# Optimization experiments

Hardware: AMD Instinct MI355X
Metric: run time of the kernel (lower is better)

Reference implementation:

```python
import jax, jax.numpy as jnp
import numpy as np

B = 256
H = W = 14
HW = H * W
TS = 0.03  # sigmoid temperature
TC = 0.07  # contrastive temperature
TP_K = int(HW * 0.1)   # 19
TN_K = int(HW * 0.5)   # 98
EPS_NORM = 1e-12
EPS_PD = 1e-6  # torch F.pairwise_distance eps


def _l2norm(x, axis):
    n = jnp.sqrt(jnp.sum(x * x, axis=axis, keepdims=True))
    return x / jnp.maximum(n, EPS_NORM)


def _conv(x, w):
    return jax.lax.conv_general_dilated(
        x, w, window_strides=(1, 1), padding='SAME',
        dimension_numbers=('NCHW', 'OIHW', 'NCHW'))


def setup_inputs() -> dict:
    key = jax.random.key(0)
    ks = jax.random.split(key, 7)
    ev = jax.random.normal(ks[0], (B, 384, H, W), dtype=jnp.float32)
    ea = jax.random.normal(ks[1], (B, 2048), dtype=jnp.float32)
    masks = jax.random.randint(ks[2], (B, H, W), 0, 2).astype(jnp.int32)
    masks = masks.at[:, 0, 0].set(1)  # guarantee nonzero mask area
    W_fc1 = jax.random.normal(ks[3], (512, 2048), dtype=jnp.float32) * 0.02
    W_fc2 = jax.random.normal(ks[4], (512, 512), dtype=jnp.float32) * 0.02
    W_conv1 = jax.random.normal(ks[5], (512, 384, 3, 3), dtype=jnp.float32) * 0.02
    W_conv2 = jax.random.normal(ks[6], (512, 512, 3, 3), dtype=jnp.float32) * 0.02
    return {'ev': ev, 'ea': ea, 'masks': masks, 'W_fc1': W_fc1,
            'W_fc2': W_fc2, 'W_conv1': W_conv1, 'W_conv2': W_conv2}


def reference(ev, ea, masks, W_fc1, W_fc2, W_conv1, W_conv2):
    # Audio_Proj: fc2(relu(fc1(ea)))  -> (B, 512)
    fa = jnp.maximum(ea @ W_fc1.T, 0.0) @ W_fc2.T

    # Visual_Proj: conv2(relu(conv1(ev))) -> (B, 512, 14, 14)
    fv_map = _conv(jnp.maximum(_conv(ev, W_conv1), 0.0), W_conv2)
    fv_map_norm = _l2norm(fv_map, axis=1)

    # masked mean pooling over the Ncut mask -> indicator vector (B, 512)
    m = masks.astype(jnp.float32)
    ind_vec = jnp.sum(fv_map * m[:, None], axis=(2, 3)) / jnp.sum(m, axis=(1, 2))[:, None]
    ind_vec_norm = _l2norm(ind_vec, axis=1)

    # Sij[i, j, p] = <fv_map_norm[i, :, p], ind_vec_norm[j]>  -> (B, B, HW)
    Sij = jnp.einsum('ichw,jc->ijhw', fv_map_norm, ind_vec_norm).reshape(B, B, HW)

    # per-row topk thresholds (kth largest / kth smallest)
    pos_thr = jax.lax.top_k(Sij, TP_K)[0][..., -1:]           # (B, B, 1)
    neg_thr = -jax.lax.top_k(-Sij, TN_K)[0][..., -1:]         # (B, B, 1)

    m_p = jax.nn.sigmoid((Sij - pos_thr) / TS)
    m_n = 1.0 - jax.nn.sigmoid((Sij - neg_thr) / TS)

    SP = jnp.sum(Sij * m_p, axis=-1) / jnp.sum(m_p, axis=-1)  # (B, B)
    SN = jnp.sum(Sij * m_n, axis=-1) / jnp.sum(m_n, axis=-1)  # (B, B)

    logits1 = jnp.concatenate([SP, SN], axis=1) / TC          # (B, 2B)
    logits2 = jnp.concatenate([SP.T, SN.T], axis=1) / TC
    labels = jnp.arange(B)
    loss1 = -jnp.mean(jax.nn.log_softmax(logits1, axis=-1)[labels, labels])
    loss2 = -jnp.mean(jax.nn.log_softmax(logits2, axis=-1)[labels, labels])

    # squared pairwise distance between detached ind_vec and fa (torch eps in diff)
    diff = jax.lax.stop_gradient(ind_vec)[:, None, :] - fa[None, :, :] + EPS_PD
    dist_mat = jnp.sum(diff * diff, axis=-1)                  # (B, B)

    ivn_d = jax.lax.stop_gradient(ind_vec_norm)
    vv_logits = ivn_d @ ivn_d.T
    eye = jnp.eye(B, dtype=jnp.float32)
    w = -vv_logits * (1.0 - eye) + eye
    dist_mat = dist_mat * w

    mask_mat = eye - (1.0 - eye) / (B - 1)
    loss3 = jnp.mean(jnp.maximum(jnp.sum(dist_mat * mask_mat, axis=1) + 0.6, 0.0))
    loss4 = jnp.mean(jnp.maximum(jnp.sum(dist_mat * mask_mat, axis=0) + 0.6, 0.0))

    return ((loss1 + loss2) / 2.0, (loss3 + loss4) / 2.0)
```

## Files before the change

### kernel.cpp

```cpp
#include <hip/hip_runtime.h>
#include <stdint.h>


typedef __attribute__((ext_vector_type(8))) short bf16x8;
typedef __attribute__((ext_vector_type(4))) float f32x4;

__device__ __forceinline__ unsigned short f2bf(float x) {
  unsigned u = __float_as_uint(x);
  unsigned r = u + 0x7FFFu + ((u >> 16) & 1u);
  return (unsigned short)(r >> 16);
}
__device__ __forceinline__ float bf2f(unsigned short h) {
  return __uint_as_float(((unsigned)h) << 16);
}

typedef const __attribute__((address_space(1))) void* gptr1_t;
typedef __attribute__((address_space(3))) void* lptr3_t;
__device__ __forceinline__ void gload_lds16(const void* g, void* l) {
  __builtin_amdgcn_global_load_lds((gptr1_t)g, (lptr3_t)l, 16, 0, 0);
}

__device__ __forceinline__ float waveSum(float v) {
#pragma unroll
  for (int m = 1; m < 64; m <<= 1) v += __shfl_xor(v, m, 64);
  return v;
}
__device__ __forceinline__ float waveMax(float v) {
#pragma unroll
  for (int m = 1; m < 64; m <<= 1) v = fmaxf(v, __shfl_xor(v, m, 64));
  return v;
}
template <int NW>
__device__ __forceinline__ float blockSum(float v) {
  __shared__ float sh[NW];
  v = waveSum(v);
  int wv = threadIdx.x >> 6, ln = threadIdx.x & 63;
  if (ln == 0) sh[wv] = v;
  __syncthreads();
  float r = 0.f;
#pragma unroll
  for (int w = 0; w < NW; ++w) r += sh[w];
  __syncthreads();
  return r;
}
template <int NW>
__device__ __forceinline__ float blockMax(float v) {
  __shared__ float sh[NW];
  v = waveMax(v);
  int wv = threadIdx.x >> 6, ln = threadIdx.x & 63;
  if (ln == 0) sh[wv] = v;
  __syncthreads();
  float r = -3.4e38f;
#pragma unroll
  for (int w = 0; w < NW; ++w) r = fmaxf(r, sh[w]);
  __syncthreads();
  return r;
}

#define RA 65536

template <int KC, int EPI>
__global__ __launch_bounds__(256, 2) void convtap6_k(
    const unsigned short* __restrict__ A, const unsigned short* __restrict__ Bw,
    unsigned short* __restrict__ C) {
  __shared__ __align__(16) short Ah[256 * 72];
  __shared__ __align__(16) short Bb[2][128 * 72];
  const int tid = threadIdx.x;
  const int wave = tid >> 6, lane = tid & 63;
  const int wm = wave >> 1, wn = wave & 1;
  const int quad = lane >> 4, tq = lane & 15;
  const int img = blockIdx.x, n0 = blockIdx.y * 128;

  int pab[7];
#pragma unroll
  for (int mi = 0; mi < 7; ++mi) {
    int p = wm * 112 + mi * 16 + tq;
    int h = p / 14, w = p - h * 14;
    int pr = (p < 196) ? ((h + 1) * 16 + w + 1) : 17;
    pab[mi] = pr * 72 + quad * 8;
  }
  int nb[4];
#pragma unroll
  for (int ni = 0; ni < 4; ++ni)
    nb[ni] = (wn * 64 + ni * 16 + tq) * 72 + quad * 8;

  const char* Ab = (const char*)A;
  const char* Bg = (const char*)Bw;
  const int l16 = lane * 16;

  f32x4 acc[7][4];
#pragma unroll
  for (int mi = 0; mi < 7; ++mi)
#pragma unroll
    for (int ni = 0; ni < 4; ++ni) {
      f32x4 z = {0.f, 0.f, 0.f, 0.f};
      acc[mi][ni] = z;
    }

  auto stageA = [&](int kc) {
    size_t s0 = ((size_t)kc * RA + img * 256) * 144;
#pragma unroll
    for (int i = 0; i < 9; ++i) {
      int c = wave + i * 4;
      gload_lds16(Ab + s0 + (size_t)c * 1024 + l16, (char*)Ah + c * 1024);
    }
  };
  auto stageB = [&](int t, int kc, int buf) {
    size_t s0 = ((size_t)(t * KC + kc) * 512 + n0) * 144;
#pragma unroll
    for (int i = 0; i < 5; ++i) {
      int c = wave + i * 4;
      if (c < 18)
        gload_lds16(Bg + s0 + (size_t)c * 1024 + l16, (char*)Bb[buf] + c * 1024);
    }
  };

  stageA(0);
  stageB(0, 0, 0);
  __syncthreads();

  const int NS = KC * 9;
#pragma unroll 1
  for (int s = 0; s < NS; ++s) {
    int kc = s / 9, t = s - kc * 9;
    if (s + 1 < NS) {
      int kc1 = (s + 1) / 9, t1 = (s + 1) - kc1 * 9;
      stageB(t1, kc1, (s + 1) & 1);
    }
    const int aoff = (((t / 3) - 1) * 16 + (t % 3) - 1) * 72;
    const short* Bc = Bb[s & 1];
#pragma unroll
    for (int h = 0; h < 2; ++h) {
      bf16x8 af[7], bf[4];
#pragma unroll
      for (int mi = 0; mi < 7; ++mi)
        af[mi] = *(const bf16x8*)&Ah[pab[mi] + aoff + h * 32];
#pragma unroll
      for (int ni = 0; ni < 4; ++ni)
        bf[ni] = *(const bf16x8*)&Bc[nb[ni] + h * 32];
#pragma unroll
      for (int mi = 0; mi < 7; ++mi)
#pragma unroll
        for (int ni = 0; ni < 4; ++ni)
          acc[mi][ni] = __builtin_amdgcn_mfma_f32_16x16x32_bf16(
              af[mi], bf[ni], acc[mi][ni], 0, 0, 0);
    }
    __syncthreads();
    if (t == 8 && kc + 1 < KC) {
      stageA(kc + 1);
      __syncthreads();
    }
  }

#pragma unroll
  for (int mi = 0; mi < 7; ++mi) {
#pragma unroll
    for (int r = 0; r < 4; ++r) {
      int p = wm * 112 + mi * 16 + quad * 4 + r;
      if (p >= 196) continue;
      int h = p / 14, w = p - h * 14;
      if (EPI == 0) {
        int cell = img * 256 + (h + 1) * 16 + w + 1;
        int slice = (n0 >> 6) + wn;
        size_t ob = ((size_t)slice * RA + cell) * 72 + tq;
#pragma unroll
        for (int ni = 0; ni < 4; ++ni)
          C[ob + ni * 16] = f2bf(fmaxf(acc[mi][ni][r], 0.f));
      } else {
        size_t ob = (size_t)(img * 196 + p) * 512 + n0 + wn * 64 + tq;
#pragma unroll
        for (int ni = 0; ni < 4; ++ni)
          C[ob + ni * 16] = f2bf(acc[mi][ni][r]);
      }
    }
  }
}

template <int K, int NLD, int EPI>
__global__ __launch_bounds__(256, 2) void gemm1_k(
    const unsigned short* __restrict__ A, const unsigned short* __restrict__ Bw,
    void* __restrict__ C, const float* __restrict__ rs) {
  __shared__ short As[128 * 64];
  __shared__ short Bs[128 * 64];
  const int tid = threadIdx.x;
  const int wave = tid >> 6, lane = tid & 63;
  const int m0 = blockIdx.x * 128, n0 = blockIdx.y * 128;
  const int rr8 = lane >> 3, seg = lane & 7, gseg = seg ^ rr8;
  const int wm = wave >> 1, wn = wave & 1;
  const int quad = lane >> 4, tq = lane & 15;

  size_t asrc[4], bsrc[4];
#pragma unroll
  for (int i8 = 0; i8 < 4; ++i8) {
    int rloc = wave * 32 + i8 * 8 + rr8;
    asrc[i8] = (size_t)(m0 + rloc) * K + gseg * 8;
    bsrc[i8] = (size_t)(n0 + rloc) * K + gseg * 8;
  }

  f32x4 acc[4][4];
#pragma unroll
  for (int mi = 0; mi < 4; ++mi)
#pragma unroll
    for (int ni = 0; ni < 4; ++ni) {
      f32x4 z = {0.f, 0.f, 0.f, 0.f};
      acc[mi][ni] = z;
    }

#pragma unroll 1
  for (int kc2 = 0; kc2 < K / 64; ++kc2) {
    int kb = kc2 * 64;
    __syncthreads();
#pragma unroll
    for (int i8 = 0; i8 < 4; ++i8) {
      gload_lds16(A + asrc[i8] + kb, &As[(wave * 32 + i8 * 8) * 64]);
      gload_lds16(Bw + bsrc[i8] + kb, &Bs[(wave * 32 + i8 * 8) * 64]);
    }
    __syncthreads();
#pragma unroll
    for (int h = 0; h < 2; ++h) {
      bf16x8 af[4], bfr[4];
#pragma unroll
      for (int mi = 0; mi < 4; ++mi) {
        int row = wm * 64 + mi * 16 + tq;
        af[mi] = *(const bf16x8*)&As[row * 64 +
                                     ((((h << 2) | quad) ^ (row & 7)) << 3)];
      }
#pragma unroll
      for (int ni = 0; ni < 4; ++ni) {
        int row = wn * 64 + ni * 16 + tq;
        bfr[ni] = *(const bf16x8*)&Bs[row * 64 +
                                      ((((h << 2) | quad) ^ (row & 7)) << 3)];
      }
#pragma unroll
      for (int mi = 0; mi < 4; ++mi)
#pragma unroll
        for (int ni = 0; ni < 4; ++ni)
          acc[mi][ni] = __builtin_amdgcn_mfma_f32_16x16x32_bf16(
              af[mi], bfr[ni], acc[mi][ni], 0, 0, 0);
    }
  }

#pragma unroll
  for (int mi = 0; mi < 4; ++mi) {
#pragma unroll
    for (int r = 0; r < 4; ++r) {
      int m = m0 + wm * 64 + mi * 16 + quad * 4 + r;
      float sc = (EPI == 3) ? rs[m] : 1.f;
      size_t obase = (size_t)m * NLD + n0 + wn * 64 + tq;
#pragma unroll
      for (int ni = 0; ni < 4; ++ni) {
        float v = acc[mi][ni][r];
        size_t idx = obase + ni * 16;
        if (EPI == 0)
          ((unsigned short*)C)[idx] = f2bf(fmaxf(v, 0.f));
        else if (EPI == 2)
          ((float*)C)[idx] = v;
        else
          ((float*)C)[idx] = v * sc;
      }
    }
  }
}

__global__ __launch_bounds__(256, 2) void gemm_xv_k(
    const unsigned short* __restrict__ ivpb, const unsigned short* __restrict__ fab,
    const unsigned short* __restrict__ indnb, float* __restrict__ Xm,
    float* __restrict__ Vm) {
  const unsigned short* A = blockIdx.z ? indnb : ivpb;
  const unsigned short* Bw = blockIdx.z ? indnb : fab;
  float* C = blockIdx.z ? Vm : Xm;
  __shared__ short As[128 * 64];
  __shared__ short Bs[128 * 64];
  const int tid = threadIdx.x;
  const int wave = tid >> 6, lane = tid & 63;
  const int m0 = blockIdx.x * 128, n0 = blockIdx.y * 128;
  const int rr8 = lane >> 3, seg = lane & 7, gseg = seg ^ rr8;
  const int wm = wave >> 1, wn = wave & 1;
  const int quad = lane >> 4, tq = lane & 15;
  size_t asrc[4], bsrc[4];
#pragma unroll
  for (int i8 = 0; i8 < 4; ++i8) {
    int rloc = wave * 32 + i8 * 8 + rr8;
    asrc[i8] = (size_t)(m0 + rloc) * 512 + gseg * 8;
    bsrc[i8] = (size_t)(n0 + rloc) * 512 + gseg * 8;
  }
  f32x4 acc[4][4];
#pragma unroll
  for (int mi = 0; mi < 4; ++mi)
#pragma unroll
    for (int ni = 0; ni < 4; ++ni) {
      f32x4 z = {0.f, 0.f, 0.f, 0.f};
      acc[mi][ni] = z;
    }
#pragma unroll 1
  for (int kc2 = 0; kc2 < 8; ++kc2) {
    int kb = kc2 * 64;
    __syncthreads();
#pragma unroll
    for (int i8 = 0; i8 < 4; ++i8) {
      gload_lds16(A + asrc[i8] + kb, &As[(wave * 32 + i8 * 8) * 64]);
      gload_lds16(Bw + bsrc[i8] + kb, &Bs[(wave * 32 + i8 * 8) * 64]);
    }
    __syncthreads();
#pragma unroll
    for (int h = 0; h < 2; ++h) {
      bf16x8 af[4], bfr[4];
#pragma unroll
      for (int mi = 0; mi < 4; ++mi) {
        int row = wm * 64 + mi * 16 + tq;
        af[mi] = *(const bf16x8*)&As[row * 64 +
                                     ((((h << 2) | quad) ^ (row & 7)) << 3)];
      }
#pragma unroll
      for (int ni = 0; ni < 4; ++ni) {
        int row = wn * 64 + ni * 16 + tq;
        bfr[ni] = *(const bf16x8*)&Bs[row * 64 +
                                      ((((h << 2) | quad) ^ (row & 7)) << 3)];
      }
#pragma unroll
      for (int mi = 0; mi < 4; ++mi)
#pragma unroll
        for (int ni = 0; ni < 4; ++ni)
          acc[mi][ni] = __builtin_amdgcn_mfma_f32_16x16x32_bf16(
              af[mi], bfr[ni], acc[mi][ni], 0, 0, 0);
    }
  }
#pragma unroll
  for (int mi = 0; mi < 4; ++mi)
#pragma unroll
    for (int r = 0; r < 4; ++r) {
      int m = m0 + wm * 64 + mi * 16 + quad * 4 + r;
      size_t obase = (size_t)m * 256 + n0 + wn * 64 + tq;
#pragma unroll
      for (int ni = 0; ni < 4; ++ni) C[obase + ni * 16] = acc[mi][ni][r];
    }
}

__global__ void prep_all_k(const float* __restrict__ ea,
                           const float* __restrict__ Wf1,
                           const float* __restrict__ Wf2,
                           const float* __restrict__ Wc1,
                           const float* __restrict__ Wc2,
                           unsigned short* __restrict__ eab,
                           unsigned short* __restrict__ wf1b,
                           unsigned short* __restrict__ wf2b,
                           unsigned short* __restrict__ wb1,
                           unsigned short* __restrict__ wb2,
                           unsigned int* __restrict__ x1u) {
  int i = blockIdx.x * 256 + threadIdx.x;
  if (i < 524288) {
    eab[i] = f2bf(ea[i]);
  } else if (i < 1572864) {
    int j = i - 524288;
    wf1b[j] = f2bf(Wf1[j]);
  } else if (i < 1835008) {
    int j = i - 1572864;
    wf2b[j] = f2bf(Wf2[j]);
  } else if (i < 3604480) {
    int j = i - 1835008;
    int t = j / (6 * 512 * 64), r = j - t * (6 * 512 * 64);
    int kc = r / (512 * 64), r2 = r - kc * (512 * 64);
    int n = r2 >> 6, c = r2 & 63;
    wb1[((size_t)(t * 6 + kc) * 512 + n) * 72 + c] =
        f2bf(Wc1[(n * 384 + kc * 64 + c) * 9 + t]);
  } else if (i < 5963776) {
    int j = i - 3604480;
    int t = j / (8 * 512 * 64), r = j - t * (8 * 512 * 64);
    int kc = r / (512 * 64), r2 = r - kc * (512 * 64);
    int n = r2 >> 6, c = r2 & 63;
    wb2[((size_t)(t * 8 + kc) * 512 + n) * 72 + c] =
        f2bf(Wc2[(n * 512 + kc * 64 + c) * 9 + t]);
  } else {
    int j = i - 5963776;
    int hr = j >> 8, u = j & 255;
    int slice = u >> 5, uu = u & 31;
    int b = hr / 60, c = hr - b * 60;
    int cell;
    if (c < 16) cell = c;
    else if (c < 32) cell = 240 + (c - 16);
    else if (c < 46) cell = (c - 31) * 16;
    else cell = (c - 45) * 16 + 15;
    x1u[((size_t)slice * RA + b * 256 + cell) * 36 + uu] = 0u;
  }
}

__global__ __launch_bounds__(256) void evpad_k(const float* __restrict__ ev,
                                               unsigned short* __restrict__ out) {
  int b = blockIdx.x, ct = blockIdx.y;
  __shared__ float tile[64][197];
  int tid = threadIdx.x;
  const float* src = ev + ((size_t)b * 384 + ct * 64) * 196;
#pragma unroll 1
  for (int it = 0; it < 49; ++it) {
    int idx = it * 256 + tid;
    int c = idx / 196, p = idx - c * 196;
    tile[c][p] = src[idx];
  }
  __syncthreads();
  unsigned short* dst = out + ((size_t)ct * RA + b * 256) * 72;
#pragma unroll 1
  for (int it = 0; it < 64; ++it) {
    int idx = it * 256 + tid;
    int cell = idx >> 6, c = idx & 63;
    int h = (cell >> 4) - 1, w = (cell & 15) - 1;
    float v = ((unsigned)h < 14u && (unsigned)w < 14u) ? tile[c][h * 14 + w]
                                                       : 0.f;
    dst[(size_t)cell * 72 + c] = f2bf(v);
  }
}


__global__ __launch_bounds__(512) void pool_k(
    const unsigned short* __restrict__ fv, const int* __restrict__ masks,
    unsigned short* __restrict__ indnb, unsigned short* __restrict__ ivpb,
    float* __restrict__ Pi, float* __restrict__ rn) {
  int b = blockIdx.x;
  int w = threadIdx.x >> 6, lane = threadIdx.x & 63;
  __shared__ float red[8][512];
  __shared__ float msh[8];
  float acc[8] = {0.f, 0.f, 0.f, 0.f, 0.f, 0.f, 0.f, 0.f};
  float msum = 0.f;
  for (int p = w; p < 196; p += 8) {
    float m = (float)masks[b * 196 + p];
    msum += m;
    uint4 d = *(const uint4*)(fv + (size_t)(b * 196 + p) * 512 + lane * 8);
    const unsigned short* hp = (const unsigned short*)&d;
    float ss = 0.f;
#pragma unroll
    for (int k = 0; k < 8; ++k) {
      float x = bf2f(hp[k]);
      ss += x * x;
      acc[k] += m * x;
    }
    ss = waveSum(ss);
    if (lane == 0) rn[b * 196 + p] = 1.f / fmaxf(sqrtf(ss), 1e-12f);
  }
#pragma unroll
  for (int k = 0; k < 8; ++k) red[w][lane * 8 + k] = acc[k];
  if (lane == 0) msh[w] = msum;
  __syncthreads();
  int tid = threadIdx.x;
  float s = 0.f, mtot = 0.f;
#pragma unroll
  for (int ww = 0; ww < 8; ++ww) {
    s += red[ww][tid];
    mtot += msh[ww];
  }
  float v = s / mtot;
  float ss2 = blockSum<8>(v * v);
  float sc = 1.f / fmaxf(sqrtf(ss2), 1e-12f);
  indnb[b * 512 + tid] = f2bf(v * sc);
  float ve = v + 1e-6f;
  ivpb[b * 512 + tid] = f2bf(ve);
  float p2 = blockSum<8>(ve * ve);
  if (tid == 0) Pi[b] = p2;
}

__global__ __launch_bounds__(512) void fanorm_k(const float* __restrict__ fa,
                                                unsigned short* __restrict__ fab,
                                                float* __restrict__ Qj) {
  int b = blockIdx.x, tid = threadIdx.x;
  float v = fa[b * 512 + tid];
  fab[b * 512 + tid] = f2bf(v);
  float q = blockSum<8>(v * v);
  if (tid == 0) Qj[b] = q;
}


__device__ __forceinline__ float radix_kth(unsigned k0, unsigned k1, unsigned k2,
                                           unsigned k3, int k) {
  unsigned prefix = 0;
  int kk = k;
#pragma unroll 1
  for (int bit = 31; bit >= 14; --bit) {
    unsigned thi = (prefix >> bit) | 1u;
    int c = __popcll(__ballot((k0 >> bit) == thi)) +
            __popcll(__ballot((k1 >> bit) == thi)) +
            __popcll(__ballot((k2 >> bit) == thi)) +
            __popcll(__ballot((k3 >> bit) == thi));
    if (kk <= c)
      prefix |= (1u << bit);
    else
      kk -= c;
  }
  unsigned u = (prefix & 0x80000000u) ? (prefix ^ 0x80000000u) : ~prefix;
  return __uint_as_float(u);
}
__device__ __forceinline__ unsigned sortkey(float x) {
  unsigned u = __float_as_uint(x);
  return u ^ (((int)u >> 31) | 0x80000000u);
}

__global__ __launch_bounds__(256) void spsn_k(const float* __restrict__ Sij,
                                              float* __restrict__ SP,
                                              float* __restrict__ SN) {
  int i = blockIdx.x, jg = blockIdx.y;
  int tid = threadIdx.x, wave = tid >> 6, lane = tid & 63;
  __shared__ float tile[196 * 65];
#pragma unroll 1
  for (int it = 0; it < 49; ++it) {
    int lin = it * 256 + tid;
    int p = lin >> 6, j = lin & 63;
    tile[p * 65 + j] = Sij[(size_t)(i * 196 + p) * 256 + jg * 64 + j];
  }
  __syncthreads();
#pragma unroll 1
  for (int jj = 0; jj < 16; ++jj) {
    int j = jj * 4 + wave;
    float v0 = tile[lane * 65 + j];
    float v1 = tile[(lane + 64) * 65 + j];
    float v2 = tile[(lane + 128) * 65 + j];
    bool val3 = lane < 4;
    float v3 = val3 ? tile[(lane + 192) * 65 + j] : 0.f;
    unsigned k0 = sortkey(v0), k1 = sortkey(v1), k2 = sortkey(v2);
    unsigned k3 = val3 ? sortkey(v3) : 0u;
    float thrP = radix_kth(k0, k1, k2, k3, 19);
    float thrN = radix_kth(k0, k1, k2, k3, 99);
    float spn = 0.f, spd = 0.f, snn = 0.f, snd = 0.f;
    const float invTS = 1.f / 0.03f;
#pragma unroll
    for (int q = 0; q < 4; ++q) {
      float v = (q == 0) ? v0 : (q == 1) ? v1 : (q == 2) ? v2 : v3;
      bool ok = (q < 3) || val3;
      if (ok) {
        float mp = 1.f / (1.f + __expf((thrP - v) * invTS));
        float mn = 1.f / (1.f + __expf((v - thrN) * invTS));
        spn += v * mp;
        spd += mp;
        snn += v * mn;
        snd += mn;
      }
    }
    spn = waveSum(spn); spd = waveSum(spd);
    snn = waveSum(snn); snd = waveSum(snd);
    if (lane == 0) {
      SP[i * 256 + jg * 64 + j] = spn / spd;
      SN[i * 256 + jg * 64 + j] = snn / snd;
    }
  }
}

__global__ __launch_bounds__(256) void loss12_k(const float* __restrict__ SP,
                                                const float* __restrict__ SN,
                                                float* __restrict__ out) {
  int r = blockIdx.x;
  int i = r & 255;
  bool col = r >= 256;
  int tid = threadIdx.x;
  const float invTC = 1.f / 0.07f;
  float a = (col ? SP[tid * 256 + i] : SP[i * 256 + tid]) * invTC;
  float b = (col ? SN[tid * 256 + i] : SN[i * 256 + tid]) * invTC;
  float mx = blockMax<4>(fmaxf(a, b));
  float se = blockSum<4>(__expf(a - mx) + __expf(b - mx));
  float lse = mx + __logf(se);
  if (tid == 0) {
    float diag = SP[i * 256 + i] * invTC;
    atomicAdd(out, -(diag - lse) * (1.f / 512.f));
  }
}

__global__ __launch_bounds__(256) void distcomb_k(
    const float* __restrict__ Pi, const float* __restrict__ Qj,
    const float* __restrict__ X, const float* __restrict__ V,
    float* __restrict__ val, float* __restrict__ out) {
  int i = blockIdx.x, j = threadIdx.x;
  float d = Pi[i] - 2.f * X[i * 256 + j] + Qj[j];
  float w = (i == j) ? 1.f : -V[i * 256 + j];
  float x = d * w;
  val[i * 256 + j] = x;
  __shared__ float diag_sh;
  if (j == i) diag_sh = x;
  float tot = blockSum<4>(x);
  if (j == 0) {
    float rs = diag_sh - (tot - diag_sh) * (1.f / 255.f);
    atomicAdd(out + 1, fmaxf(rs + 0.6f, 0.f) * (1.f / 512.f));
  }
}

__global__ __launch_bounds__(256) void loss4_k(const float* __restrict__ val,
                                               float* __restrict__ out) {
  int j = blockIdx.x, i = threadIdx.x;
  float x = val[i * 256 + j];
  __shared__ float diag_sh;
  if (i == j) diag_sh = x;
  float tot = blockSum<4>(x);
  if (i == 0) {
    float cs = diag_sh - (tot - diag_sh) * (1.f / 255.f);
    atomicAdd(out + 1, fmaxf(cs + 0.6f, 0.f) * (1.f / 512.f));
  }
}


extern "C" void kernel_launch(void* const* d_in, const int* in_sizes, int n_in,
                              void* d_out, int out_size, void* d_ws,
                              size_t ws_size, hipStream_t stream) {
  (void)in_sizes; (void)n_in; (void)out_size; (void)ws_size;
  const float* ev = (const float*)d_in[0];
  const float* ea = (const float*)d_in[1];
  const int* msk = (const int*)d_in[2];
  const float* Wf1 = (const float*)d_in[3];
  const float* Wf2 = (const float*)d_in[4];
  const float* Wc1 = (const float*)d_in[5];
  const float* Wc2 = (const float*)d_in[6];
  float* out = (float*)d_out;
  char* ws = (char*)d_ws;

  size_t off = 0;
  auto alloc = [&](size_t bytes) {
    void* p = ws + off;
    off = (off + bytes + 255) & ~(size_t)255;
    return p;
  };
  unsigned short* evb = (unsigned short*)alloc((size_t)6 * RA * 144);
  unsigned short* fv = evb;
  unsigned short* x1b = (unsigned short*)alloc((size_t)8 * RA * 144);
  float* Sij = (float*)x1b;
  unsigned short* wb1 = (unsigned short*)alloc((size_t)9 * 6 * 512 * 144);
  unsigned short* wb2 = (unsigned short*)alloc((size_t)9 * 8 * 512 * 144);
  unsigned short* eab = (unsigned short*)alloc((size_t)256 * 2048 * 2);
  unsigned short* wf1b = (unsigned short*)alloc((size_t)512 * 2048 * 2);
  unsigned short* wf2b = (unsigned short*)alloc((size_t)512 * 512 * 2);
  unsigned short* hb = (unsigned short*)alloc((size_t)256 * 512 * 2);
  float* fa = (float*)alloc((size_t)256 * 512 * 4);
  unsigned short* indnb = (unsigned short*)alloc((size_t)256 * 512 * 2);
  unsigned short* ivpb = (unsigned short*)alloc((size_t)256 * 512 * 2);
  unsigned short* fab = (unsigned short*)alloc((size_t)256 * 512 * 2);
  float* Pi = (float*)alloc(256 * 4);
  float* Qj = (float*)alloc(256 * 4);
  float* Xm = (float*)alloc((size_t)256 * 256 * 4);
  float* Vm = (float*)alloc((size_t)256 * 256 * 4);
  float* rn = (float*)alloc((size_t)50176 * 4);
  float* SP = (float*)alloc((size_t)256 * 256 * 4);
  float* SN = (float*)alloc((size_t)256 * 256 * 4);
  float* val = (float*)alloc((size_t)256 * 256 * 4);

  hipMemsetAsync(out, 0, 2 * sizeof(float), stream);

  prep_all_k<<<38656, 256, 0, stream>>>(ea, Wf1, Wf2, Wc1, Wc2, eab, wf1b,
                                        wf2b, wb1, wb2, (unsigned int*)x1b);
  evpad_k<<<dim3(256, 6), 256, 0, stream>>>(ev, evb);

  convtap6_k<6, 0><<<dim3(256, 4), 256, 0, stream>>>(evb, wb1, x1b);
  gemm1_k<2048, 512, 0><<<dim3(2, 4), 256, 0, stream>>>(eab, wf1b, hb, nullptr);
  gemm1_k<512, 512, 2><<<dim3(2, 4), 256, 0, stream>>>(hb, wf2b, fa, nullptr);
  convtap6_k<8, 1><<<dim3(256, 4), 256, 0, stream>>>(x1b, wb2, fv);

  pool_k<<<256, 512, 0, stream>>>(fv, msk, indnb, ivpb, Pi, rn);
  fanorm_k<<<256, 512, 0, stream>>>(fa, fab, Qj);

  gemm1_k<512, 256, 3><<<dim3(392, 2), 256, 0, stream>>>(fv, indnb, Sij, rn);
  gemm_xv_k<<<dim3(2, 2, 2), 256, 0, stream>>>(ivpb, fab, indnb, Xm, Vm);

  spsn_k<<<dim3(256, 4), 256, 0, stream>>>(Sij, SP, SN);
  loss12_k<<<512, 256, 0, stream>>>(SP, SN, out);
  distcomb_k<<<256, 256, 0, stream>>>(Pi, Qj, Xm, Vm, val, out);
  loss4_k<<<256, 256, 0, stream>>>(val, out);
}
```

Before: 852.0 us.

## Load conv weight fragments directly into registers and use padded-row M indexing

The conv kernels stop staging weight tiles through double-buffered LDS. Each wave now reads its B fragments straight from global memory into a two-slot register buffer, prefetching the next tap while the current one computes, and the weight layout is packed to 64 columns. The M dimension now indexes padded 16-wide rows directly, which removes the per-pixel div/mod and computes 224 rows instead of 196, with columns 14 and 15 skipped at output. This removes most per-tap barriers and frees LDS, at the cost of redundant global/L2 weight reads across waves and blocks and more VGPR use.

```diff
diff --git a/kernel.cpp b/kernel.cpp
--- a/kernel.cpp
+++ b/kernel.cpp
@@ -60,11 +60,10 @@
 #define RA 65536
 
 template <int KC, int EPI>
-__global__ __launch_bounds__(256, 2) void convtap6_k(
+__global__ __launch_bounds__(256, 2) void convtap7_k(
     const unsigned short* __restrict__ A, const unsigned short* __restrict__ Bw,
     unsigned short* __restrict__ C) {
-  __shared__ __align__(16) short Ah[256 * 72];
-  __shared__ __align__(16) short Bb[2][128 * 72];
+  __shared__ __align__(16) short Ah[258 * 72];
   const int tid = threadIdx.x;
   const int wave = tid >> 6, lane = tid & 63;
   const int wm = wave >> 1, wn = wave & 1;
@@ -73,19 +72,15 @@
 
   int pab[7];
 #pragma unroll
-  for (int mi = 0; mi < 7; ++mi) {
-    int p = wm * 112 + mi * 16 + tq;
-    int h = p / 14, w = p - h * 14;
-    int pr = (p < 196) ? ((h + 1) * 16 + w + 1) : 17;
-    pab[mi] = pr * 72 + quad * 8;
-  }
-  int nb[4];
+  for (int mi = 0; mi < 7; ++mi)
+    pab[mi] = (wm * 112 + mi * 16 + tq + 17) * 72 + quad * 8;
+
+  int brow64[4];
 #pragma unroll
   for (int ni = 0; ni < 4; ++ni)
-    nb[ni] = (wn * 64 + ni * 16 + tq) * 72 + quad * 8;
+    brow64[ni] = (n0 + wn * 64 + ni * 16 + tq) * 64 + quad * 8;
 
   const char* Ab = (const char*)A;
-  const char* Bg = (const char*)Bw;
   const int l16 = lane * 16;
 
   f32x4 acc[7][4];
@@ -97,6 +92,8 @@
       acc[mi][ni] = z;
     }
 
+  bf16x8 breg[2][8];
+
   auto stageA = [&](int kc) {
     size_t s0 = ((size_t)kc * RA + img * 256) * 144;
 #pragma unroll
@@ -105,49 +102,43 @@
       gload_lds16(Ab + s0 + (size_t)c * 1024 + l16, (char*)Ah + c * 1024);
     }
   };
-  auto stageB = [&](int t, int kc, int buf) {
-    size_t s0 = ((size_t)(t * KC + kc) * 512 + n0) * 144;
-#pragma unroll
-    for (int i = 0; i < 5; ++i) {
-      int c = wave + i * 4;
-      if (c < 18)
-        gload_lds16(Bg + s0 + (size_t)c * 1024 + l16, (char*)Bb[buf] + c * 1024);
-    }
+  auto loadB = [&](int t, int kc, bf16x8* dst) {
+    const unsigned short* slab = Bw + (size_t)(t * KC + kc) * 32768;
+#pragma unroll
+    for (int ni = 0; ni < 4; ++ni)
+#pragma unroll
+      for (int h = 0; h < 2; ++h)
+        dst[ni * 2 + h] = *(const bf16x8*)(slab + brow64[ni] + h * 32);
   };
 
   stageA(0);
-  stageB(0, 0, 0);
-  __syncthreads();
-
-  const int NS = KC * 9;
-#pragma unroll 1
-  for (int s = 0; s < NS; ++s) {
-    int kc = s / 9, t = s - kc * 9;
-    if (s + 1 < NS) {
-      int kc1 = (s + 1) / 9, t1 = (s + 1) - kc1 * 9;
-      stageB(t1, kc1, (s + 1) & 1);
-    }
-    const int aoff = (((t / 3) - 1) * 16 + (t % 3) - 1) * 72;
-    const short* Bc = Bb[s & 1];
-#pragma unroll
-    for (int h = 0; h < 2; ++h) {
-      bf16x8 af[7], bf[4];
-#pragma unroll
-      for (int mi = 0; mi < 7; ++mi)
-        af[mi] = *(const bf16x8*)&Ah[pab[mi] + aoff + h * 32];
-#pragma unroll
-      for (int ni = 0; ni < 4; ++ni)
-        bf[ni] = *(const bf16x8*)&Bc[nb[ni] + h * 32];
-#pragma unroll
-      for (int mi = 0; mi < 7; ++mi)
-#pragma unroll
-        for (int ni = 0; ni < 4; ++ni)
-          acc[mi][ni] = __builtin_amdgcn_mfma_f32_16x16x32_bf16(
-              af[mi], bf[ni], acc[mi][ni], 0, 0, 0);
-    }
-    __syncthreads();
-    if (t == 8 && kc + 1 < KC) {
+  loadB(0, 0, breg[0]);
+  __syncthreads();
+
+#pragma unroll 1
+  for (int kc = 0; kc < KC; ++kc) {
+#pragma unroll
+    for (int t = 0; t < 9; ++t) {
+      if (t < 8) loadB(t + 1, kc, breg[(t + 1) & 1]);
+      const int aoff = (((t / 3) - 1) * 16 + (t % 3) - 1) * 72;
+#pragma unroll
+      for (int h = 0; h < 2; ++h) {
+        bf16x8 af[7];
+#pragma unroll
+        for (int mi = 0; mi < 7; ++mi)
+          af[mi] = *(const bf16x8*)&Ah[pab[mi] + aoff + h * 32];
+#pragma unroll
+        for (int mi = 0; mi < 7; ++mi)
+#pragma unroll
+          for (int ni = 0; ni < 4; ++ni)
+            acc[mi][ni] = __builtin_amdgcn_mfma_f32_16x16x32_bf16(
+                af[mi], breg[t & 1][ni * 2 + h], acc[mi][ni], 0, 0, 0);
+      }
+    }
+    if (kc + 1 < KC) {
+      __syncthreads();
       stageA(kc + 1);
+      loadB(0, kc + 1, breg[0]);
       __syncthreads();
     }
   }
@@ -156,18 +147,19 @@
   for (int mi = 0; mi < 7; ++mi) {
 #pragma unroll
     for (int r = 0; r < 4; ++r) {
-      int p = wm * 112 + mi * 16 + quad * 4 + r;
-      if (p >= 196) continue;
-      int h = p / 14, w = p - h * 14;
+      int lr = wm * 112 + mi * 16 + quad * 4 + r;
+      int w = lr & 15;
+      if (w >= 14) continue;
+      int h = lr >> 4;
       if (EPI == 0) {
-        int cell = img * 256 + (h + 1) * 16 + w + 1;
+        int cell = img * 256 + lr + 17;
         int slice = (n0 >> 6) + wn;
         size_t ob = ((size_t)slice * RA + cell) * 72 + tq;
 #pragma unroll
         for (int ni = 0; ni < 4; ++ni)
           C[ob + ni * 16] = f2bf(fmaxf(acc[mi][ni][r], 0.f));
       } else {
-        size_t ob = (size_t)(img * 196 + p) * 512 + n0 + wn * 64 + tq;
+        size_t ob = (size_t)(img * 196 + h * 14 + w) * 512 + n0 + wn * 64 + tq;
 #pragma unroll
         for (int ni = 0; ni < 4; ++ni)
           C[ob + ni * 16] = f2bf(acc[mi][ni][r]);
@@ -361,15 +353,13 @@
     int t = j / (6 * 512 * 64), r = j - t * (6 * 512 * 64);
     int kc = r / (512 * 64), r2 = r - kc * (512 * 64);
     int n = r2 >> 6, c = r2 & 63;
-    wb1[((size_t)(t * 6 + kc) * 512 + n) * 72 + c] =
-        f2bf(Wc1[(n * 384 + kc * 64 + c) * 9 + t]);
+    wb1[j] = f2bf(Wc1[(n * 384 + kc * 64 + c) * 9 + t]);
   } else if (i < 5963776) {
     int j = i - 3604480;
     int t = j / (8 * 512 * 64), r = j - t * (8 * 512 * 64);
     int kc = r / (512 * 64), r2 = r - kc * (512 * 64);
     int n = r2 >> 6, c = r2 & 63;
-    wb2[((size_t)(t * 8 + kc) * 512 + n) * 72 + c] =
-        f2bf(Wc2[(n * 512 + kc * 64 + c) * 9 + t]);
+    wb2[j] = f2bf(Wc2[(n * 512 + kc * 64 + c) * 9 + t]);
   } else {
     int j = i - 5963776;
     int hr = j >> 8, u = j & 255;
@@ -615,8 +605,8 @@
   unsigned short* fv = evb;
   unsigned short* x1b = (unsigned short*)alloc((size_t)8 * RA * 144);
   float* Sij = (float*)x1b;
-  unsigned short* wb1 = (unsigned short*)alloc((size_t)9 * 6 * 512 * 144);
-  unsigned short* wb2 = (unsigned short*)alloc((size_t)9 * 8 * 512 * 144);
+  unsigned short* wb1 = (unsigned short*)alloc((size_t)9 * 6 * 512 * 128);
+  unsigned short* wb2 = (unsigned short*)alloc((size_t)9 * 8 * 512 * 128);
   unsigned short* eab = (unsigned short*)alloc((size_t)256 * 2048 * 2);
   unsigned short* wf1b = (unsigned short*)alloc((size_t)512 * 2048 * 2);
   unsigned short* wf2b = (unsigned short*)alloc((size_t)512 * 512 * 2);
@@ -640,10 +630,10 @@
                                         wf2b, wb1, wb2, (unsigned int*)x1b);
   evpad_k<<<dim3(256, 6), 256, 0, stream>>>(ev, evb);
 
-  convtap6_k<6, 0><<<dim3(256, 4), 256, 0, stream>>>(evb, wb1, x1b);
+  convtap7_k<6, 0><<<dim3(256, 4), 256, 0, stream>>>(evb, wb1, x1b);
   gemm1_k<2048, 512, 0><<<dim3(2, 4), 256, 0, stream>>>(eab, wf1b, hb, nullptr);
   gemm1_k<512, 512, 2><<<dim3(2, 4), 256, 0, stream>>>(hb, wf2b, fa, nullptr);
-  convtap6_k<8, 1><<<dim3(256, 4), 256, 0, stream>>>(x1b, wb2, fv);
+  convtap7_k<8, 1><<<dim3(256, 4), 256, 0, stream>>>(x1b, wb2, fv);
 
   pool_k<<<256, 512, 0, stream>>>(fv, msk, indnb, ivpb, Pi, rn);
   fanorm_k<<<256, 512, 0, stream>>>(fa, fab, Qj);
```

Result: slower. 923.5 us (+8.4%).
